# Performance work log

Hardware: AMD Instinct MI355X
Metric: run time of the kernel (lower is better)

Reference implementation:

```python
import jax, jax.numpy as jnp
import numpy as np


def setup_inputs() -> dict:
    key = jax.random.key(0)
    k1, k2, k3 = jax.random.split(key, 3)
    B, L, D = 4, 4096, 1024
    inputs = jax.random.normal(k1, (B, L, D), dtype=jnp.float32)
    # nn.Linear(2D, 2D): weight [out=2D, in=2D], bias [2D]
    W_gate = jax.random.normal(k2, (2 * D, 2 * D), dtype=jnp.float32) * (1.0 / np.sqrt(2 * D))
    b_gate = jax.random.normal(k3, (2 * D,), dtype=jnp.float32) * 0.01
    return {"inputs": inputs, "W_gate": W_gate, "b_gate": b_gate}


def reference(inputs, W_gate, b_gate):
    B, L, D = inputs.shape
    # Cumulative average: tril(ones)/arange mask matmul == prefix-mean (linear time)
    denom = jnp.arange(1, L + 1, dtype=inputs.dtype)[None, :, None]  # [1, L, 1]
    average_outputs = jnp.cumsum(inputs, axis=1) / denom  # [B, L, D]
    # Gating linear on concat(inputs, avg): y = x @ W^T + b
    cat = jnp.concatenate([inputs, average_outputs], axis=-1)  # [B, L, 2D]
    gating = jnp.einsum('bld,ed->ble', cat, W_gate) + b_gate  # [B, L, 2D]
    input_gate, forget_gate = jnp.split(gating, 2, axis=-1)
    gating_outputs = (jax.nn.sigmoid(input_gate) * inputs
                      + jax.nn.sigmoid(forget_gate) * average_outputs)
    return gating_outputs, average_outputs
```

## Files before the change

kernel.cpp:

```cpp
#include <hip/hip_runtime.h>

#define B_   4
#define L_   4096
#define D_   1024
#define ROWS (B_ * L_)
#define K2   (2 * D_)
#define BLD  (ROWS * D_)
#define CH   128
#define NC   32

typedef __attribute__((ext_vector_type(8))) short s8v;
typedef __attribute__((ext_vector_type(4))) float f4v;

__device__ __forceinline__ unsigned short f2bf(float f) {
    unsigned int u = __float_as_uint(f);
    u += 0x7FFFu + ((u >> 16) & 1u);
    return (unsigned short)(u >> 16);
}

__device__ __forceinline__ float sigmoidf_(float v) {
    return 1.0f / (1.0f + __expf(-v));
}

__device__ __forceinline__ void llds16(const void* g, void* l) {
    __builtin_amdgcn_global_load_lds(
        (const __attribute__((address_space(1))) unsigned int*)(g),
        (__attribute__((address_space(3))) unsigned int*)(l),
        16, 0, 0);
}


__global__ void partial_sums(const float* __restrict__ x, float* __restrict__ part) {
    int bid  = blockIdx.x;
    int dblk = bid & 3;
    int c    = (bid >> 2) & 31;
    int b    = bid >> 7;
    int d    = dblk * 256 + threadIdx.x;
    const float* p = x + ((size_t)(b * L_ + c * CH) * D_ + d);
    float s = 0.f;
#pragma unroll 8
    for (int i = 0; i < CH; ++i) s += p[(size_t)i * D_];
    part[(b * NC + c) * D_ + d] = s;
}

__global__ void scan_chunks(float* __restrict__ part) {
    int idx = blockIdx.x * 256 + threadIdx.x;
    int b = idx >> 10, d = idx & 1023;
    float run = 0.f;
#pragma unroll
    for (int c = 0; c < NC; ++c) {
        int o = (b * NC + c) * D_ + d;
        float t = part[o];
        part[o] = run;
        run += t;
    }
}

__global__ void apply_scan(const float* __restrict__ x, const float* __restrict__ part,
                           float* __restrict__ avg_out, unsigned short* __restrict__ Abf) {
    int bid  = blockIdx.x;
    int dblk = bid & 3;
    int c    = (bid >> 2) & 31;
    int b    = bid >> 7;
    int d    = dblk * 256 + threadIdx.x;
    size_t row0 = (size_t)b * L_ + (size_t)c * CH;
    const float* p = x + (row0 * D_ + d);
    float s = part[(b * NC + c) * D_ + d];
    for (int i = 0; i < CH; ++i) {
        size_t row = row0 + i;
        float xi = p[(size_t)i * D_];
        s += xi;
        float av = s / (float)(c * CH + i + 1);
        avg_out[row * D_ + d]      = av;
        Abf[row * K2 + d]          = f2bf(xi);
        Abf[row * K2 + D_ + d]     = f2bf(av);
    }
}

__global__ void conv_w(const float4* __restrict__ W, ushort4* __restrict__ Wbf) {
    int t = blockIdx.x * 256 + threadIdx.x;
    float4 v = W[t];
    ushort4 o;
    o.x = f2bf(v.x); o.y = f2bf(v.y); o.z = f2bf(v.z); o.w = f2bf(v.w);
    Wbf[t] = o;
}

__global__ __launch_bounds__(256, 2) void gemm_gated(
        const unsigned short* __restrict__ Abf, const unsigned short* __restrict__ Wbf,
        const float* __restrict__ x, const float* __restrict__ avg,
        const float* __restrict__ bg, float* __restrict__ out) {
    __shared__ __attribute__((aligned(16))) unsigned short sA [128 * 32];
    __shared__ __attribute__((aligned(16))) unsigned short sB0[128 * 32];
    __shared__ __attribute__((aligned(16))) unsigned short sB1[128 * 32];

    const int t    = threadIdx.x;
    const int w    = t >> 6;
    const int lane = t & 63;
    const int bid  = blockIdx.x;
    const int tileN = bid & 7, tileM = bid >> 3;
    const int row0 = tileM * 128, col0 = tileN * 128;
    const int wm = w >> 1, wn = w & 1;
    const int quad = lane >> 4, lcol = lane & 15;

    f4v acc0[4][4], acc1[4][4];
#pragma unroll
    for (int i = 0; i < 4; ++i)
#pragma unroll
        for (int j = 0; j < 4; ++j)
#pragma unroll
            for (int r = 0; r < 4; ++r) { acc0[i][j][r] = 0.f; acc1[i][j][r] = 0.f; }

    const int c0 = t, c1 = 256 + t;
    const unsigned short* gA0 = Abf + ((size_t)(row0 + (c0 >> 2)) * K2 + (c0 & 3) * 8);
    const unsigned short* gA1 = Abf + ((size_t)(row0 + (c1 >> 2)) * K2 + (c1 & 3) * 8);
    const unsigned short* gB0a = Wbf + ((size_t)(col0 + (c0 >> 2)) * K2 + (c0 & 3) * 8);
    const unsigned short* gB0b = Wbf + ((size_t)(col0 + (c1 >> 2)) * K2 + (c1 & 3) * 8);
    const unsigned short* gB1a = Wbf + ((size_t)(col0 + 1024 + (c0 >> 2)) * K2 + (c0 & 3) * 8);
    const unsigned short* gB1b = Wbf + ((size_t)(col0 + 1024 + (c1 >> 2)) * K2 + (c1 & 3) * 8);
    unsigned short* lA0  = &sA [w * 512];
    unsigned short* lA1  = &sA [2048 + w * 512];
    unsigned short* lB0a = &sB0[w * 512];
    unsigned short* lB0b = &sB0[2048 + w * 512];
    unsigned short* lB1a = &sB1[w * 512];
    unsigned short* lB1b = &sB1[2048 + w * 512];

    for (int k0 = 0; k0 < K2; k0 += 32) {
        __syncthreads();
        llds16(gA0  + k0, lA0);
        llds16(gA1  + k0, lA1);
        llds16(gB0a + k0, lB0a);
        llds16(gB0b + k0, lB0b);
        llds16(gB1a + k0, lB1a);
        llds16(gB1b + k0, lB1b);
        __syncthreads();

        s8v af[4], bf0[4], bf1[4];
#pragma unroll
        for (int i = 0; i < 4; ++i)
            af[i] = *(const s8v*)&sA[(wm * 64 + i * 16 + lcol) * 32 + quad * 8];
#pragma unroll
        for (int j = 0; j < 4; ++j) {
            bf0[j] = *(const s8v*)&sB0[(wn * 64 + j * 16 + lcol) * 32 + quad * 8];
            bf1[j] = *(const s8v*)&sB1[(wn * 64 + j * 16 + lcol) * 32 + quad * 8];
        }
#pragma unroll
        for (int i = 0; i < 4; ++i)
#pragma unroll
            for (int j = 0; j < 4; ++j) {
                acc0[i][j] = __builtin_amdgcn_mfma_f32_16x16x32_bf16(af[i], bf0[j], acc0[i][j], 0, 0, 0);
                acc1[i][j] = __builtin_amdgcn_mfma_f32_16x16x32_bf16(af[i], bf1[j], acc1[i][j], 0, 0, 0);
            }
    }

    float b1v[4], b2v[4];
#pragma unroll
    for (int j = 0; j < 4; ++j) {
        int cc = col0 + wn * 64 + j * 16 + lcol;
        b1v[j] = bg[cc];
        b2v[j] = bg[1024 + cc];
    }
#pragma unroll
    for (int i = 0; i < 4; ++i) {
#pragma unroll
        for (int j = 0; j < 4; ++j) {
            int rr = row0 + wm * 64 + i * 16 + quad * 4;
            int cc = col0 + wn * 64 + j * 16 + lcol;
#pragma unroll
            for (int r = 0; r < 4; ++r) {
                size_t off = (size_t)(rr + r) * D_ + cc;
                float gi = sigmoidf_(acc0[i][j][r] + b1v[j]);
                float gf = sigmoidf_(acc1[i][j][r] + b2v[j]);
                out[off] = gi * x[off] + gf * avg[off];
            }
        }
    }
}

extern "C" void kernel_launch(void* const* d_in, const int* in_sizes, int n_in,
                              void* d_out, int out_size, void* d_ws, size_t ws_size,
                              hipStream_t stream) {
    const float* x  = (const float*)d_in[0];
    const float* W  = (const float*)d_in[1];
    const float* bg = (const float*)d_in[2];
    float* out = (float*)d_out;
    float* avg = out + (size_t)BLD;

    char* ws = (char*)d_ws;
    unsigned short* Abf = (unsigned short*)(ws);
    unsigned short* Wbf = (unsigned short*)(ws + (size_t)67108864);
    float*          prt = (float*)(ws + (size_t)75497472);

    conv_w<<<dim3(4096), dim3(256), 0, stream>>>((const float4*)W, (ushort4*)Wbf);
    partial_sums<<<dim3(512), dim3(256), 0, stream>>>(x, prt);
    scan_chunks<<<dim3(16), dim3(256), 0, stream>>>(prt);
    apply_scan<<<dim3(512), dim3(256), 0, stream>>>(x, prt, avg, Abf);
    gemm_gated<<<dim3(1024), dim3(256), 0, stream>>>(Abf, Wbf, x, avg, bg, out);
}
```

Measured before the change: 397.8 us.

## Vectorize prefix-mean kernels and fold chunk scan into apply pass

Rewrites the partial-sum and apply kernels to process float4 columns per thread and write bf16 operands as ushort4. The separate chunk-scan kernel is removed; each apply block instead sums the preceding chunk partials itself, with chunk size halved to 64 for more chunks. Division is replaced by a shared reciprocal table. This reduces narrow 2-byte stores and one launch, at the cost of redundant partial summation in later chunks and fewer blocks.

```diff
diff --git a/kernel.cpp b/kernel.cpp
--- a/kernel.cpp
+++ b/kernel.cpp
@@ -6,8 +6,8 @@
 #define ROWS (B_ * L_)
 #define K2   (2 * D_)
 #define BLD  (ROWS * D_)
-#define CH   128
-#define NC   32
+#define CH   64
+#define NC   64
 
 typedef __attribute__((ext_vector_type(8))) short s8v;
 typedef __attribute__((ext_vector_type(4))) float f4v;
@@ -30,50 +30,50 @@
 }
 
 
-__global__ void partial_sums(const float* __restrict__ x, float* __restrict__ part) {
-    int bid  = blockIdx.x;
-    int dblk = bid & 3;
-    int c    = (bid >> 2) & 31;
-    int b    = bid >> 7;
-    int d    = dblk * 256 + threadIdx.x;
-    const float* p = x + ((size_t)(b * L_ + c * CH) * D_ + d);
-    float s = 0.f;
+__global__ void partial_sums(const float4* __restrict__ x4, float4* __restrict__ part4) {
+    int bid = blockIdx.x;
+    int c = bid & 63, b = bid >> 6;
+    int t = threadIdx.x;
+    const float4* p = x4 + ((size_t)(b * L_ + c * CH) * 256 + t);
+    float4 s; s.x = 0.f; s.y = 0.f; s.z = 0.f; s.w = 0.f;
 #pragma unroll 8
-    for (int i = 0; i < CH; ++i) s += p[(size_t)i * D_];
-    part[(b * NC + c) * D_ + d] = s;
+    for (int i = 0; i < CH; ++i) {
+        float4 v = p[(size_t)i * 256];
+        s.x += v.x; s.y += v.y; s.z += v.z; s.w += v.w;
+    }
+    part4[(size_t)bid * 256 + t] = s;
 }
 
-__global__ void scan_chunks(float* __restrict__ part) {
-    int idx = blockIdx.x * 256 + threadIdx.x;
-    int b = idx >> 10, d = idx & 1023;
-    float run = 0.f;
-#pragma unroll
-    for (int c = 0; c < NC; ++c) {
-        int o = (b * NC + c) * D_ + d;
-        float t = part[o];
-        part[o] = run;
-        run += t;
+__global__ void apply_scan(const float4* __restrict__ x4, const float4* __restrict__ part4,
+                           float4* __restrict__ avg4, ushort4* __restrict__ A4) {
+    __shared__ float inv[CH];
+    int bid = blockIdx.x;
+    int c = bid & 63, b = bid >> 6;
+    int t = threadIdx.x;
+    if (t < CH) inv[t] = 1.0f / (float)(c * CH + t + 1);
+
+    float4 s; s.x = 0.f; s.y = 0.f; s.z = 0.f; s.w = 0.f;
+    for (int cc = 0; cc < c; ++cc) {
+        float4 v = part4[((size_t)(b * NC + cc)) * 256 + t];
+        s.x += v.x; s.y += v.y; s.z += v.z; s.w += v.w;
     }
-}
+    __syncthreads();
 
-__global__ void apply_scan(const float* __restrict__ x, const float* __restrict__ part,
-                           float* __restrict__ avg_out, unsigned short* __restrict__ Abf) {
-    int bid  = blockIdx.x;
-    int dblk = bid & 3;
-    int c    = (bid >> 2) & 31;
-    int b    = bid >> 7;
-    int d    = dblk * 256 + threadIdx.x;
     size_t row0 = (size_t)b * L_ + (size_t)c * CH;
-    const float* p = x + (row0 * D_ + d);
-    float s = part[(b * NC + c) * D_ + d];
+    const float4* px = x4 + (row0 * 256 + t);
+    float4*       pa = avg4 + (row0 * 256 + t);
+    ushort4*      pA = A4 + (row0 * 512 + t);
+#pragma unroll 4
     for (int i = 0; i < CH; ++i) {
-        size_t row = row0 + i;
-        float xi = p[(size_t)i * D_];
-        s += xi;
-        float av = s / (float)(c * CH + i + 1);
-        avg_out[row * D_ + d]      = av;
-        Abf[row * K2 + d]          = f2bf(xi);
-        Abf[row * K2 + D_ + d]     = f2bf(av);
+        float4 v = px[(size_t)i * 256];
+        s.x += v.x; s.y += v.y; s.z += v.z; s.w += v.w;
+        float r = inv[i];
+        float4 av; av.x = s.x * r; av.y = s.y * r; av.z = s.z * r; av.w = s.w * r;
+        pa[(size_t)i * 256] = av;
+        ushort4 ux; ux.x = f2bf(v.x);  ux.y = f2bf(v.y);  ux.z = f2bf(v.z);  ux.w = f2bf(v.w);
+        ushort4 ua; ua.x = f2bf(av.x); ua.y = f2bf(av.y); ua.z = f2bf(av.z); ua.w = f2bf(av.w);
+        pA[(size_t)i * 512]       = ux;
+        pA[(size_t)i * 512 + 256] = ua;
     }
 }
 
@@ -188,11 +188,11 @@
     char* ws = (char*)d_ws;
     unsigned short* Abf = (unsigned short*)(ws);
     unsigned short* Wbf = (unsigned short*)(ws + (size_t)67108864);
-    float*          prt = (float*)(ws + (size_t)75497472);
+    float4* prt4 = (float4*)(ws + (size_t)67108864);
 
+    partial_sums<<<dim3(256), dim3(256), 0, stream>>>((const float4*)x, prt4);
+    apply_scan<<<dim3(256), dim3(256), 0, stream>>>((const float4*)x, prt4,
+                                                    (float4*)avg, (ushort4*)Abf);
     conv_w<<<dim3(4096), dim3(256), 0, stream>>>((const float4*)W, (ushort4*)Wbf);
-    partial_sums<<<dim3(512), dim3(256), 0, stream>>>(x, prt);
-    scan_chunks<<<dim3(16), dim3(256), 0, stream>>>(prt);
-    apply_scan<<<dim3(512), dim3(256), 0, stream>>>(x, prt, avg, Abf);
     gemm_gated<<<dim3(1024), dim3(256), 0, stream>>>(Abf, Wbf, x, avg, bg, out);
 }
```

Result: faster. 379.8 us (-4.5%).
